# Kernel optimization log

Hardware: AMD Instinct MI355X
Metric: run time of the kernel (lower is better)

The kernel has to match this reference:

```python
import jax, jax.numpy as jnp
import numpy as np

NUM_EXPERTS = 8
TOP_K = 2
BALANCE_LOSS_COEF = 0.01


def setup_inputs() -> dict:
    key = jax.random.key(0)
    ks = jax.random.split(key, 5)
    B, S, H, I, E = 8, 2048, 512, 2048, NUM_EXPERTS
    return {
        "hidden_states": jax.random.normal(ks[0], (B, S, H), dtype=jnp.float32),
        "Wg": jax.random.normal(ks[1], (H, E), dtype=jnp.float32) * (1.0 / np.sqrt(H)),
        "bg": jnp.zeros((E,), dtype=jnp.float32),
        "W1": jax.random.normal(ks[2], (E, H, I), dtype=jnp.float32) * (1.0 / np.sqrt(H)),
        "b1": jnp.zeros((E, I), dtype=jnp.float32),
        "W2": jax.random.normal(ks[3], (E, I, H), dtype=jnp.float32) * (1.0 / np.sqrt(I)),
        "b2": jnp.zeros((E, H), dtype=jnp.float32),
    }


def reference(hidden_states, Wg, bg, W1, b1, W2, b2):
    B, S, H = hidden_states.shape
    E, K = NUM_EXPERTS, TOP_K

    # ---- Router: softmax gate + top-k, renormalized weights ----
    logits = jnp.einsum('bsh,he->bse', hidden_states, Wg) + bg       # [B,S,E]
    probs = jax.nn.softmax(logits, axis=-1)                          # [B,S,E]
    top_p, top_i = jax.lax.top_k(probs, K)                           # [B,S,K]
    routing_weights = top_p / jnp.sum(top_p, axis=-1, keepdims=True)  # [B,S,K]

    # ---- Experts: compute every expert densely (small fixed E), then gather ----
    h = jnp.einsum('bsh,ehi->ebsi', hidden_states, W1) + b1[:, None, None, :]
    h = jax.nn.gelu(h)
    y = jnp.einsum('ebsi,eih->ebsh', h, W2) + b2[:, None, None, :]   # [E,B,S,H]

    y = jnp.moveaxis(y, 0, 2)                                        # [B,S,E,H]
    sel = jnp.take_along_axis(y, top_i[..., None], axis=2)           # [B,S,K,H]
    output = jnp.sum(routing_weights[..., None] * sel, axis=2) + hidden_states

    # ---- Load balancing loss (Switch-style): E * sum_e f_e * P_e ----
    assign = jnp.sum(jax.nn.one_hot(top_i, E, dtype=probs.dtype), axis=2)  # [B,S,E]
    f = jnp.mean(assign, axis=(0, 1)) / K                            # fraction dispatched
    P = jnp.mean(probs, axis=(0, 1))                                 # mean router prob
    balance_loss = BALANCE_LOSS_COEF * E * jnp.sum(f * P)

    return output, balance_loss
```

## Files before the change

### kernel.cpp

```cpp
#include <hip/hip_runtime.h>

#define BS_TOK 16384
#define HD 512
#define IDIM 2048
#define NE 8
#define RT_MAX 264
#define CAP (RT_MAX * 128)

typedef unsigned short u16;
typedef unsigned int u32;
typedef __attribute__((ext_vector_type(8))) __bf16 bf16x8;
typedef __attribute__((ext_vector_type(4))) float f32x4;

__device__ __forceinline__ u16 f2bf(float f) {
  u32 u = __builtin_bit_cast(u32, f);
  u += 0x7fffu + ((u >> 16) & 1u);
  return (u16)(u >> 16);
}
__device__ __forceinline__ u16 f2bf_hw(float f) {
  u32 r;
  asm("v_cvt_pk_bf16_f32 %0, %1, %2" : "=v"(r) : "v"(f), "v"(f));
  return (u16)r;
}
__device__ __forceinline__ float bflo(u32 u) { return __builtin_bit_cast(float, u << 16); }
__device__ __forceinline__ float bfhi(u32 u) { return __builtin_bit_cast(float, u & 0xffff0000u); }
__device__ __forceinline__ float gelu_t(float v) {
  float t = v * (-2.302558f - 0.1029474f * v * v);
  return v * __builtin_amdgcn_rcpf(1.0f + __builtin_amdgcn_exp2f(t));
}
__device__ __forceinline__ void gload16(const u16* g, u16* l) {
  __builtin_amdgcn_global_load_lds((const __attribute__((address_space(1))) u16*)g,
                                   (__attribute__((address_space(3))) u16*)l, 16, 0, 0);
}

__global__ void k_prep(const float* __restrict__ W1, u16* __restrict__ W1T,
                       const float* __restrict__ W2, u16* __restrict__ W2T,
                       const float* __restrict__ x, const float* __restrict__ Wg,
                       const float* __restrict__ bg, int* __restrict__ top_e,
                       float* __restrict__ top_w, u32* __restrict__ counts,
                       float* __restrict__ Psum, u16* __restrict__ xb) {
  int bid = blockIdx.x;
  int tid = threadIdx.x;
  if (bid < 16384) {
    __shared__ float t[32][33];
    int z = bid >> 10, rem = bid & 1023;
    int gy = rem >> 6, gx = rem & 63;
    const float* in; u16* out; int R, C, bx, by;
    if (z < NE) { in = W1; out = W1T; R = HD; C = IDIM; bx = gx; by = gy; }
    else { in = W2; out = W2T; R = IDIM; C = HD; bx = gy; by = gx; z -= NE; }
    size_t eb = (size_t)z * HD * IDIM;
    int c0 = bx * 32, r0 = by * 32;
    int tx = tid & 31, ty = tid >> 5;
    #pragma unroll
    for (int j = ty; j < 32; j += 8) t[j][tx] = in[eb + (size_t)(r0 + j) * C + (c0 + tx)];
    __syncthreads();
    #pragma unroll
    for (int j = ty; j < 32; j += 8) out[eb + (size_t)(c0 + j) * R + (r0 + tx)] = f2bf_hw(t[tx][j]);
    return;
  }
  __shared__ float wg_s[HD * NE];
  __shared__ float Pp[NE];
  __shared__ u32 cnt[NE];
  if (tid < NE) { Pp[tid] = 0.f; cnt[tid] = 0; }
  for (int i = tid; i < HD * NE; i += 256) wg_s[i] = Wg[i];
  __syncthreads();
  int wv = tid >> 6, lane = tid & 63;
  int t = (bid - 16384) * 4 + wv;
  const float4* xr = (const float4*)(x + (size_t)t * HD + lane * 8);
  float4 a = xr[0], b = xr[1];
  u32 p0 = f2bf(a.x) | ((u32)f2bf(a.y) << 16);
  u32 p1 = f2bf(a.z) | ((u32)f2bf(a.w) << 16);
  u32 p2 = f2bf(b.x) | ((u32)f2bf(b.y) << 16);
  u32 p3 = f2bf(b.z) | ((u32)f2bf(b.w) << 16);
  ((uint4*)(xb + (size_t)t * HD))[lane] = make_uint4(p0, p1, p2, p3);

  float acc[NE];
  #pragma unroll
  for (int e = 0; e < NE; ++e) acc[e] = 0.f;
  #pragma unroll
  for (int j = 0; j < 8; ++j) {
    float xv = j < 4 ? (&a.x)[j] : (&b.x)[j - 4];
    int hh = lane * 8 + j;
    #pragma unroll
    for (int e = 0; e < NE; ++e) acc[e] += xv * wg_s[hh * NE + e];
  }
  #pragma unroll
  for (int off = 32; off > 0; off >>= 1) {
    #pragma unroll
    for (int e = 0; e < NE; ++e) acc[e] += __shfl_down(acc[e], off);
  }
  if (lane == 0) {
    float lg[NE];
    #pragma unroll
    for (int e = 0; e < NE; ++e) lg[e] = acc[e] + bg[e];
    int i1 = 0; float m1 = lg[0];
    #pragma unroll
    for (int e = 1; e < NE; ++e) if (lg[e] > m1) { m1 = lg[e]; i1 = e; }
    int i2 = -1; float m2 = -1e30f;
    #pragma unroll
    for (int e = 0; e < NE; ++e) if (e != i1 && lg[e] > m2) { m2 = lg[e]; i2 = e; }
    float s = 0.f, p[NE];
    #pragma unroll
    for (int e = 0; e < NE; ++e) { p[e] = __expf(lg[e] - m1); s += p[e]; }
    float inv = 1.f / s;
    #pragma unroll
    for (int e = 0; e < NE; ++e) { p[e] *= inv; atomicAdd(&Pp[e], p[e]); }
    float denom = p[i1] + p[i2];
    top_e[2 * t] = i1; top_e[2 * t + 1] = i2;
    top_w[2 * t] = p[i1] / denom; top_w[2 * t + 1] = p[i2] / denom;
    atomicAdd(&cnt[i1], 1u); atomicAdd(&cnt[i2], 1u);
  }
  __syncthreads();
  if (tid < NE) { atomicAdd(&counts[tid], cnt[tid]); atomicAdd(&Psum[tid], Pp[tid]); }
}

__global__ void k_scatter(const int* __restrict__ top_e, const float* __restrict__ top_w,
                          const u32* __restrict__ counts, const float* __restrict__ Psum,
                          u32* __restrict__ pos_rel, int* __restrict__ perm_t,
                          float* __restrict__ perm_w, u32* __restrict__ padoff,
                          int* __restrict__ inv, float* __restrict__ out) {
  __shared__ u32 po[NE];
  if (threadIdx.x == 0) {
    u32 off = 0; float loss = 0.f;
    for (int e = 0; e < NE; ++e) {
      po[e] = off;
      off += ((counts[e] + 127u) / 128u) * 128u;
      loss += ((float)counts[e] / (float)(BS_TOK * 2)) * (Psum[e] / (float)BS_TOK);
    }
    if (blockIdx.x == 0) {
      for (int e = 0; e < NE; ++e) padoff[e] = po[e];
      padoff[NE] = off;
      out[(size_t)BS_TOK * HD] = 0.01f * (float)NE * loss;
    }
  }
  __syncthreads();
  int g = blockIdx.x * 256 + threadIdx.x;
  int e = top_e[g]; float wgt = top_w[g];
  int lane = threadIdx.x & 63;
  #pragma unroll
  for (int ee = 0; ee < NE; ++ee) {
    unsigned long long m = __ballot(e == ee);
    if (e == ee) {
      int nb = __popcll(m & ((1ull << lane) - 1ull));
      int leader = __ffsll((unsigned long long)m) - 1;
      u32 base = 0;
      if (lane == leader) base = atomicAdd(&pos_rel[ee], (u32)__popcll(m));
      base = __shfl(base, leader);
      int slot = (int)(po[ee] + base) + nb;
      perm_t[slot] = g >> 1;
      perm_w[slot] = wgt;
      inv[g] = slot;
    }
  }
}

template <int KSTEPS, int NCT, int NTOT, bool GATHER, bool ACT>
__global__ __launch_bounds__(256, 2) void k_gemm(
    const u16* __restrict__ A, int lda, const u16* __restrict__ W,
    const float* __restrict__ bias, const int* __restrict__ perm_t,
    const u32* __restrict__ padoff, u16* __restrict__ C) {
  __shared__ u16 As[2][8192], Bs[2][8192];
  int nb = gridDim.x;
  int b = blockIdx.x;
  int tile = (b & 7) * (nb >> 3) + (b >> 3);
  int rt = tile / NCT, ct = tile % NCT;
  u32 s0 = (u32)rt * 128u;
  if (s0 >= padoff[NE]) return;
  int e = 0;
  #pragma unroll
  for (int k = 1; k < NE; ++k) e += (s0 >= padoff[k]) ? 1 : 0;

  int tid = threadIdx.x;
  int wv = tid >> 6, lane = tid & 63;
  int l15 = lane & 15, lg4 = lane >> 4;
  int wr = wv >> 1, wc = wv & 1;

  int srow = tid >> 3;
  int cb = (tid & 7) * 16;
  int cbs = (cb ^ ((srow & 7) << 4)) >> 1;

  const u16* ap[4]; const u16* bp[4];
  #pragma unroll
  for (int i = 0; i < 4; ++i) {
    int r = i * 32 + srow;
    int arow = GATHER ? perm_t[s0 + r] : (int)(s0 + r);
    ap[i] = A + (size_t)arow * lda + cbs;
    bp[i] = W + ((size_t)e * NTOT + ct * 128 + r) * (KSTEPS * 64) + cbs;
  }

  int base_n = ct * 128 + wc * 64;
  f32x4 acc[4][4];
  #pragma unroll
  for (int j = 0; j < 4; ++j) {
    float bv = bias[e * NTOT + base_n + j * 16 + l15];
    #pragma unroll
    for (int i = 0; i < 4; ++i) acc[i][j] = f32x4{bv, bv, bv, bv};
  }

  #pragma unroll
  for (int i = 0; i < 4; ++i) gload16(ap[i], As[0] + tid * 8 + i * 2048);
  #pragma unroll
  for (int i = 0; i < 4; ++i) gload16(bp[i], Bs[0] + tid * 8 + i * 2048);
  #pragma unroll
  for (int i = 0; i < 4; ++i) gload16(ap[i] + 64, As[1] + tid * 8 + i * 2048);
  #pragma unroll
  for (int i = 0; i < 4; ++i) gload16(bp[i] + 64, Bs[1] + tid * 8 + i * 2048);
  asm volatile("s_waitcnt vmcnt(8)" ::: "memory");
  __builtin_amdgcn_sched_barrier(0);
  __builtin_amdgcn_s_barrier();

  for (int ks = 0; ks < KSTEPS; ++ks) {
    int cur = ks & 1;
    const u16* Ab = As[cur];
    const u16* Bb = Bs[cur];
    bf16x8 af[2][4], bf[2][4];
    #pragma unroll
    for (int kk = 0; kk < 2; ++kk) {
      #pragma unroll
      for (int f = 0; f < 4; ++f) {
        int ra = wr * 64 + f * 16 + l15;
        af[kk][f] = *(const bf16x8*)((const char*)Ab +
                    (ra * 128 + ((kk * 64 + lg4 * 16) ^ ((ra & 7) << 4))));
        int rb = wc * 64 + f * 16 + l15;
        bf[kk][f] = *(const bf16x8*)((const char*)Bb +
                    (rb * 128 + ((kk * 64 + lg4 * 16) ^ ((rb & 7) << 4))));
      }
    }
    asm volatile("s_waitcnt lgkmcnt(0)" ::: "memory");
    __builtin_amdgcn_sched_barrier(0);
    __builtin_amdgcn_s_barrier();

    if (ks + 2 < KSTEPS) {
      int k0 = (ks + 2) * 64;
      #pragma unroll
      for (int i = 0; i < 4; ++i) gload16(ap[i] + k0, As[cur] + tid * 8 + i * 2048);
      #pragma unroll
      for (int i = 0; i < 4; ++i) gload16(bp[i] + k0, Bs[cur] + tid * 8 + i * 2048);
    }

    __builtin_amdgcn_s_setprio(1);
    #pragma unroll
    for (int kk = 0; kk < 2; ++kk)
      #pragma unroll
      for (int i = 0; i < 4; ++i)
        #pragma unroll
        for (int j = 0; j < 4; ++j)
          acc[i][j] = __builtin_amdgcn_mfma_f32_16x16x32_bf16(af[kk][i], bf[kk][j], acc[i][j], 0, 0, 0);
    __builtin_amdgcn_s_setprio(0);

    if (ks + 1 < KSTEPS) {
      if (ks + 2 < KSTEPS) {
        asm volatile("s_waitcnt vmcnt(8)" ::: "memory");
      } else {
        asm volatile("s_waitcnt vmcnt(0)" ::: "memory");
      }
      __builtin_amdgcn_sched_barrier(0);
      __builtin_amdgcn_s_barrier();
    }
  }

  #pragma unroll
  for (int i = 0; i < 4; ++i) {
    u32 mrow = s0 + wr * 64 + i * 16 + lg4 * 4;
    #pragma unroll
    for (int rr = 0; rr < 4; ++rr) {
      u32 m = mrow + rr;
      #pragma unroll
      for (int j = 0; j < 4; ++j) {
        float v = acc[i][j][rr];
        if (ACT) v = gelu_t(v);
        C[(size_t)m * NTOT + base_n + j * 16 + l15] = f2bf_hw(v);
      }
    }
  }
}

__global__ void k_final(const float* __restrict__ x, const u16* __restrict__ y,
                        const int* __restrict__ inv, const float* __restrict__ top_w,
                        float* __restrict__ out) {
  int tid = threadIdx.x;
  int t = blockIdx.x * 4 + (tid >> 6);
  int lane = tid & 63;
  int s0 = inv[2 * t], s1 = inv[2 * t + 1];
  float w0 = top_w[2 * t], w1 = top_w[2 * t + 1];
  size_t xo = (size_t)t * HD + lane * 8;
  float4 a = *(const float4*)(x + xo);
  float4 b = *(const float4*)(x + xo + 4);
  uint4 ya = *(const uint4*)(y + (size_t)s0 * HD + lane * 8);
  uint4 yb = *(const uint4*)(y + (size_t)s1 * HD + lane * 8);
  float4 o0, o1;
  o0.x = a.x + w0 * bflo(ya.x) + w1 * bflo(yb.x);
  o0.y = a.y + w0 * bfhi(ya.x) + w1 * bfhi(yb.x);
  o0.z = a.z + w0 * bflo(ya.y) + w1 * bflo(yb.y);
  o0.w = a.w + w0 * bfhi(ya.y) + w1 * bfhi(yb.y);
  o1.x = b.x + w0 * bflo(ya.z) + w1 * bflo(yb.z);
  o1.y = b.y + w0 * bfhi(ya.z) + w1 * bfhi(yb.z);
  o1.z = b.z + w0 * bflo(ya.w) + w1 * bflo(yb.w);
  o1.w = b.w + w0 * bfhi(ya.w) + w1 * bfhi(yb.w);
  *(float4*)(out + xo) = o0;
  *(float4*)(out + xo + 4) = o1;
}

extern "C" void kernel_launch(void* const* d_in, const int* in_sizes, int n_in,
                              void* d_out, int out_size, void* d_ws, size_t ws_size,
                              hipStream_t stream) {
  const float* x  = (const float*)d_in[0];
  const float* Wg = (const float*)d_in[1];
  const float* bg = (const float*)d_in[2];
  const float* W1 = (const float*)d_in[3];
  const float* b1 = (const float*)d_in[4];
  const float* W2 = (const float*)d_in[5];
  const float* b2 = (const float*)d_in[6];
  float* out = (float*)d_out;

  char* w = (char*)d_ws;
  u32* counts   = (u32*)(w + 0);
  u32* pos_rel  = (u32*)(w + 32);
  float* Psum   = (float*)(w + 64);
  u32* padoff   = (u32*)(w + 96);
  int* top_e    = (int*)(w + 256);
  float* top_w  = (float*)(w + 256 + 131072);
  int* invm     = (int*)(w + 256 + 2 * 131072);
  int* perm_t   = (int*)(w + 256 + 3 * 131072);
  float* perm_w = (float*)(w + 256 + 3 * 131072 + 135168);
  u16* xb  = (u16*)(w + 663808);
  u16* W1T = (u16*)(w + 17441024);
  u16* W2T = (u16*)(w + 34218240);
  u16* h   = (u16*)(w + 50995456);
  u16* y   = (u16*)(w + 189407488);
  if (ws_size < 224010496ull) return;

  (void)hipMemsetAsync(w, 0, 663808, stream);
  k_prep<<<20480, 256, 0, stream>>>(W1, W1T, W2, W2T, x, Wg, bg,
                                    top_e, top_w, counts, Psum, xb);
  k_scatter<<<(BS_TOK * 2) / 256, 256, 0, stream>>>(top_e, top_w, counts, Psum,
                                                    pos_rel, perm_t, perm_w, padoff,
                                                    invm, out);
  k_gemm<8, 16, IDIM, true, true><<<RT_MAX * 16, 256, 0, stream>>>(
      xb, HD, W1T, b1, perm_t, padoff, h);
  k_gemm<32, 4, HD, false, false><<<RT_MAX * 4, 256, 0, stream>>>(
      h, IDIM, W2T, b2, perm_t, padoff, y);
  k_final<<<BS_TOK / 4, 256, 0, stream>>>(x, y, invm, top_w, out);
}
```

Measured before the change: 359.0 us.

## Split prep kernel into wide-tile weight transpose and separate router kernel

Splits the fused prep kernel into a weight transpose/convert kernel and a router kernel. The transpose now uses 64x64 tiles with float4 loads and packed bf16 pair stores via v_cvt_pk_bf16_f32, aiming to cut global memory transactions when converting W1/W2 (about 64MB of fp32 read). The router pads the gate-weight shared array to stride 9 to avoid LDS bank conflicts and reads x with a coalesced lane stride for the dot product, at the cost of an extra kernel launch and re-reading x from global/cache. The bf16 conversion of x switches to hardware packed conversion.

```diff
diff --git a/kernel.cpp b/kernel.cpp
--- a/kernel.cpp
+++ b/kernel.cpp
@@ -9,6 +9,7 @@
 
 typedef unsigned short u16;
 typedef unsigned int u32;
+typedef unsigned long long u64;
 typedef __attribute__((ext_vector_type(8))) __bf16 bf16x8;
 typedef __attribute__((ext_vector_type(4))) float f32x4;
 
@@ -21,6 +22,11 @@
   u32 r;
   asm("v_cvt_pk_bf16_f32 %0, %1, %2" : "=v"(r) : "v"(f), "v"(f));
   return (u16)r;
+}
+__device__ __forceinline__ u32 pack2bf(float a, float b) {
+  u32 r;
+  asm("v_cvt_pk_bf16_f32 %0, %1, %2" : "=v"(r) : "v"(a), "v"(b));
+  return r;
 }
 __device__ __forceinline__ float bflo(u32 u) { return __builtin_bit_cast(float, u << 16); }
 __device__ __forceinline__ float bfhi(u32 u) { return __builtin_bit_cast(float, u & 0xffff0000u); }
@@ -33,45 +39,54 @@
                                    (__attribute__((address_space(3))) u16*)l, 16, 0, 0);
 }
 
-__global__ void k_prep(const float* __restrict__ W1, u16* __restrict__ W1T,
-                       const float* __restrict__ W2, u16* __restrict__ W2T,
-                       const float* __restrict__ x, const float* __restrict__ Wg,
-                       const float* __restrict__ bg, int* __restrict__ top_e,
-                       float* __restrict__ top_w, u32* __restrict__ counts,
-                       float* __restrict__ Psum, u16* __restrict__ xb) {
-  int bid = blockIdx.x;
+__global__ __launch_bounds__(256) void k_transW(const float* __restrict__ W1, u16* __restrict__ W1T,
+                                                const float* __restrict__ W2, u16* __restrict__ W2T) {
+  __shared__ float t[64][65];
+  int z = blockIdx.y;
+  const float* in; u16* out; int Rin, Cin;
+  if (z < NE) { in = W1; out = W1T; Rin = HD; Cin = IDIM; }
+  else { in = W2; out = W2T; Rin = IDIM; Cin = HD; z -= NE; }
+  size_t eb = (size_t)z * HD * IDIM;
+  int tpr = Cin >> 6;
+  int r0 = (blockIdx.x / tpr) << 6, c0 = (blockIdx.x % tpr) << 6;
   int tid = threadIdx.x;
-  if (bid < 16384) {
-    __shared__ float t[32][33];
-    int z = bid >> 10, rem = bid & 1023;
-    int gy = rem >> 6, gx = rem & 63;
-    const float* in; u16* out; int R, C, bx, by;
-    if (z < NE) { in = W1; out = W1T; R = HD; C = IDIM; bx = gx; by = gy; }
-    else { in = W2; out = W2T; R = IDIM; C = HD; bx = gy; by = gx; z -= NE; }
-    size_t eb = (size_t)z * HD * IDIM;
-    int c0 = bx * 32, r0 = by * 32;
-    int tx = tid & 31, ty = tid >> 5;
-    #pragma unroll
-    for (int j = ty; j < 32; j += 8) t[j][tx] = in[eb + (size_t)(r0 + j) * C + (c0 + tx)];
-    __syncthreads();
-    #pragma unroll
-    for (int j = ty; j < 32; j += 8) out[eb + (size_t)(c0 + j) * R + (r0 + tx)] = f2bf_hw(t[tx][j]);
-    return;
-  }
-  __shared__ float wg_s[HD * NE];
+  int row = tid >> 4, c4 = (tid & 15) << 2;
+  #pragma unroll
+  for (int i = 0; i < 4; ++i) {
+    float4 v = *(const float4*)(in + eb + (size_t)(r0 + row + i * 16) * Cin + c0 + c4);
+    t[row + i * 16][c4 + 0] = v.x; t[row + i * 16][c4 + 1] = v.y;
+    t[row + i * 16][c4 + 2] = v.z; t[row + i * 16][c4 + 3] = v.w;
+  }
+  __syncthreads();
+  int cc = tid >> 4, rr = (tid & 15) << 2;
+  #pragma unroll
+  for (int i = 0; i < 4; ++i) {
+    int c = cc + i * 16;
+    u32 lo = pack2bf(t[rr + 0][c], t[rr + 1][c]);
+    u32 hi = pack2bf(t[rr + 2][c], t[rr + 3][c]);
+    *(u32*)(out + eb + (size_t)(c0 + c) * Rin + r0 + rr)     = lo;
+    *(u32*)(out + eb + (size_t)(c0 + c) * Rin + r0 + rr + 2) = hi;
+  }
+}
+
+__global__ void k_router(const float* __restrict__ x, const float* __restrict__ Wg,
+                         const float* __restrict__ bg, int* __restrict__ top_e,
+                         float* __restrict__ top_w, u32* __restrict__ counts,
+                         float* __restrict__ Psum, u16* __restrict__ xb) {
+  __shared__ float wg_s[HD * 9];
   __shared__ float Pp[NE];
   __shared__ u32 cnt[NE];
+  int tid = threadIdx.x;
   if (tid < NE) { Pp[tid] = 0.f; cnt[tid] = 0; }
-  for (int i = tid; i < HD * NE; i += 256) wg_s[i] = Wg[i];
+  for (int i = tid; i < HD * NE; i += 256) wg_s[(i >> 3) * 9 + (i & 7)] = Wg[i];
   __syncthreads();
   int wv = tid >> 6, lane = tid & 63;
-  int t = (bid - 16384) * 4 + wv;
+  int t = blockIdx.x * 4 + wv;
+
   const float4* xr = (const float4*)(x + (size_t)t * HD + lane * 8);
   float4 a = xr[0], b = xr[1];
-  u32 p0 = f2bf(a.x) | ((u32)f2bf(a.y) << 16);
-  u32 p1 = f2bf(a.z) | ((u32)f2bf(a.w) << 16);
-  u32 p2 = f2bf(b.x) | ((u32)f2bf(b.y) << 16);
-  u32 p3 = f2bf(b.z) | ((u32)f2bf(b.w) << 16);
+  u32 p0 = pack2bf(a.x, a.y), p1 = pack2bf(a.z, a.w);
+  u32 p2 = pack2bf(b.x, b.y), p3 = pack2bf(b.z, b.w);
   ((uint4*)(xb + (size_t)t * HD))[lane] = make_uint4(p0, p1, p2, p3);
 
   float acc[NE];
@@ -79,10 +94,11 @@
   for (int e = 0; e < NE; ++e) acc[e] = 0.f;
   #pragma unroll
   for (int j = 0; j < 8; ++j) {
-    float xv = j < 4 ? (&a.x)[j] : (&b.x)[j - 4];
-    int hh = lane * 8 + j;
-    #pragma unroll
-    for (int e = 0; e < NE; ++e) acc[e] += xv * wg_s[hh * NE + e];
+    int h = lane + 64 * j;
+    float xv = x[(size_t)t * HD + h];
+    const float* wrow = wg_s + h * 9;
+    #pragma unroll
+    for (int e = 0; e < NE; ++e) acc[e] += xv * wrow[e];
   }
   #pragma unroll
   for (int off = 32; off > 0; off >>= 1) {
@@ -331,8 +347,8 @@
   if (ws_size < 224010496ull) return;
 
   (void)hipMemsetAsync(w, 0, 663808, stream);
-  k_prep<<<20480, 256, 0, stream>>>(W1, W1T, W2, W2T, x, Wg, bg,
-                                    top_e, top_w, counts, Psum, xb);
+  k_transW<<<dim3(256, 16), 256, 0, stream>>>(W1, W1T, W2, W2T);
+  k_router<<<BS_TOK / 4, 256, 0, stream>>>(x, Wg, bg, top_e, top_w, counts, Psum, xb);
   k_scatter<<<(BS_TOK * 2) / 256, 256, 0, stream>>>(top_e, top_w, counts, Psum,
                                                     pos_rel, perm_t, perm_w, padoff,
                                                     invm, out);
```

New measurement: 340.9 us. 5.1% less time.
